# Kernel optimization log

Hardware: AMD Instinct MI355X
Metric: run time of the kernel (lower is better)

The kernel has to match this reference:

```python
import jax, jax.numpy as jnp
import numpy as np

B, S, D, H = 64, 512, 544, 1024  # batch, seq, state_dim+pb_dim, n_hid


def setup_inputs() -> dict:
    key = jax.random.key(0)
    k_x, k_wih, k_whh, k_bih, k_bhh = jax.random.split(key, 5)
    bound = 1.0 / np.sqrt(H)  # PyTorch LSTM uniform init range
    X = jax.random.normal(k_x, (B, S, D), dtype=jnp.float32)
    W_ih = jax.random.uniform(k_wih, (4 * H, D), jnp.float32, -bound, bound)
    W_hh = jax.random.uniform(k_whh, (4 * H, H), jnp.float32, -bound, bound)
    b_ih = jax.random.uniform(k_bih, (4 * H,), jnp.float32, -bound, bound)
    b_hh = jax.random.uniform(k_bhh, (4 * H,), jnp.float32, -bound, bound)
    return {"X": X, "W_ih": W_ih, "W_hh": W_hh, "b_ih": b_ih, "b_hh": b_hh}


def reference(X, W_ih, W_hh, b_ih, b_hh):
    # Faithful to PBRNN.forward: LSTM scanned over the sequence dim
    # (the torch code loops one timestep at a time; the math is a plain
    # single-layer LSTM from zero initial state). Returns final (h, c)
    # stacked as [2, B, H] — the only state forward() produces.
    n_batch = X.shape[0]
    n_hid = W_hh.shape[1]
    Xs = jnp.swapaxes(X, 0, 1)  # [S, B, D]
    # Precompute input projections for all timesteps: [S, B, 4H]
    x_proj = jnp.einsum('sbd,gd->sbg', Xs, W_ih) + (b_ih + b_hh)

    def step(carry, xp):
        h, c = carry
        gates = xp + h @ W_hh.T  # [B, 4H]
        i, f, g, o = jnp.split(gates, 4, axis=-1)  # PyTorch gate order i,f,g,o
        i = jax.nn.sigmoid(i)
        f = jax.nn.sigmoid(f)
        g = jnp.tanh(g)
        o = jax.nn.sigmoid(o)
        c = f * c + i * g
        h = o * jnp.tanh(c)
        return (h, c), None

    h0 = jnp.zeros((n_batch, n_hid), dtype=X.dtype)
    c0 = jnp.zeros((n_batch, n_hid), dtype=X.dtype)
    (h_n, c_n), _ = jax.lax.scan(step, (h0, c0), x_proj)
    return jnp.stack([h_n, c_n])  # [2, B, H]
```

## Files before the change

kernel.cpp:

```cpp
#include <hip/hip_runtime.h>
#include <hip/hip_bf16.h>


#define B_  64
#define S_  512
#define D_  544
#define H_  1024
#define CG_ 64
#define BG_ 4
#define GRID_ (CG_*BG_)

typedef __attribute__((ext_vector_type(8))) short bf16x8;
typedef __attribute__((ext_vector_type(4))) float f32x4;

__device__ inline ushort f2b(float x){
  unsigned u = __float_as_uint(x);
  u = (u + 0x7FFFu + ((u >> 16) & 1u)) >> 16;
  return (ushort)u;
}

__device__ inline bf16x8 pack8(float4 a, float4 b){
  bf16x8 r;
  r[0]=(short)f2b(a.x); r[1]=(short)f2b(a.y); r[2]=(short)f2b(a.z); r[3]=(short)f2b(a.w);
  r[4]=(short)f2b(b.x); r[5]=(short)f2b(b.y); r[6]=(short)f2b(b.z); r[7]=(short)f2b(b.w);
  return r;
}

__device__ inline unsigned long long ld64a(const unsigned long long* q){
  return __hip_atomic_load(q, __ATOMIC_RELAXED, __HIP_MEMORY_SCOPE_AGENT);
}

__device__ inline float sigm(float x){ return __builtin_amdgcn_rcpf(1.f + __expf(-x)); }
__device__ inline float tanh_(float x){ return 1.f - 2.f*__builtin_amdgcn_rcpf(1.f + __expf(2.f*x)); }

__global__ void cvt_x(const float* __restrict__ x, ushort* __restrict__ xb, int n4){
  int i = blockIdx.x*256 + threadIdx.x;
  if (i >= n4) return;
  float4 v = ((const float4*)x)[i];
  ushort4 o;
  o.x=f2b(v.x); o.y=f2b(v.y); o.z=f2b(v.z); o.w=f2b(v.w);
  ((ushort4*)xb)[i] = o;
}

__global__ __launch_bounds__(256,1) void lstm_persist(
    const float* __restrict__ Wih, const float* __restrict__ Whh,
    const float* __restrict__ bih, const float* __restrict__ bhh,
    const ushort* __restrict__ Xb,
    unsigned* thbuf,
    float* __restrict__ out)
{
  const int tid  = threadIdx.x;
  const int wave = tid >> 6;
  const int lane = tid & 63;
  const int c16  = lane & 15;
  const int quad = lane >> 4;
  const int cg   = blockIdx.x & (CG_-1);
  const int bg   = blockIdx.x >> 6;

  __shared__ float gates_s[4][64][17];

  bf16x8 whhf[4][8];
  #pragma unroll
  for (int mt = 0; mt < 4; ++mt){
    const size_t grow = (size_t)(mt*H_ + cg*16 + c16);
    #pragma unroll
    for (int i = 0; i < 8; ++i){
      int k = wave*256 + i*32 + quad*8;
      const float4* p = (const float4*)(Whh + grow*H_ + k);
      whhf[mt][i] = pack8(p[0], p[1]);
    }
  }
  bf16x8 wihf[4][5];
  #pragma unroll
  for (int mt = 0; mt < 4; ++mt){
    const size_t grow = (size_t)(mt*H_ + cg*16 + c16);
    #pragma unroll
    for (int ii = 0; ii < 5; ++ii){
      int it = wave + 4*ii;
      if (it < 17){
        int k = it*32 + quad*8;
        const float4* p = (const float4*)(Wih + grow*D_ + k);
        wihf[mt][ii] = pack8(p[0], p[1]);
      }
    }
  }

  const int uu = tid & 15;
  const int nn = tid >> 4;
  float bsum[4];
  #pragma unroll
  for (int g = 0; g < 4; ++g)
    bsum[g] = bih[g*H_ + cg*16 + uu] + bhh[g*H_ + cg*16 + uu];
  float cstate = 0.f;

  f32x4 acc[4];

  auto zacc = [&]{
    #pragma unroll
    for (int mt = 0; mt < 4; ++mt) acc[mt] = (f32x4){0.f,0.f,0.f,0.f};
  };
  auto xp_gemm = [&](int t){
    #pragma unroll
    for (int ii = 0; ii < 5; ++ii){
      int it = wave + 4*ii;
      if (it < 17){
        int k = it*32 + quad*8;
        bf16x8 b = *(const bf16x8*)(Xb + ((size_t)(bg*16 + c16)*S_ + t)*D_ + k);
        #pragma unroll
        for (int mt = 0; mt < 4; ++mt)
          acc[mt] = __builtin_amdgcn_mfma_f32_16x16x32_bf16(wihf[mt][ii], b, acc[mt], 0,0,0);
      }
    }
  };

  zacc();
  xp_gemm(0);

  const int obase = (bg*64 + wave*16 + (quad>>1))*256 + c16*16 + (quad&1)*8;

  for (int t = 0; t < S_; ++t){
    const unsigned* hp = thbuf + (t & 1) * (B_*H_);
    unsigned*       hn = thbuf + ((t & 1) ^ 1) * (B_*H_);

    {
      const unsigned tag = (unsigned)t & 0xffffu;
      const unsigned long long tmask = 0xffff0000ffff0000ull;
      const unsigned long long texp  = ((unsigned long long)tag << 16)
                                     | ((unsigned long long)tag << 48);
      unsigned long long q[8][4];
      #pragma unroll
      for (int i = 0; i < 8; ++i){
        const unsigned long long* p = (const unsigned long long*)(hp + obase + i*512);
        q[i][0] = ld64a(p);   q[i][1] = ld64a(p+1);
        q[i][2] = ld64a(p+2); q[i][3] = ld64a(p+3);
      }
      #pragma unroll
      for (int i = 0; i < 8; ++i){
        const unsigned long long* p = (const unsigned long long*)(hp + obase + i*512);
        long guard = 0;
        while ((((q[i][0]^texp)|(q[i][1]^texp)|(q[i][2]^texp)|(q[i][3]^texp)) & tmask) != 0ull){
          q[i][0] = ld64a(p);   q[i][1] = ld64a(p+1);
          q[i][2] = ld64a(p+2); q[i][3] = ld64a(p+3);
          if (++guard > (1L<<20)) break;
        }
        union { unsigned u[4]; bf16x8 v8; } eb;
        #pragma unroll
        for (int w = 0; w < 4; ++w){
          unsigned lo = (unsigned)q[i][w];
          unsigned hi = (unsigned)(q[i][w] >> 32);
          eb.u[w] = (lo & 0xffffu) | (hi << 16);
        }
        #pragma unroll
        for (int mt = 0; mt < 4; ++mt)
          acc[mt] = __builtin_amdgcn_mfma_f32_16x16x32_bf16(whhf[mt][i], eb.v8, acc[mt], 0,0,0);
      }
    }

    #pragma unroll
    for (int mt = 0; mt < 4; ++mt)
      #pragma unroll
      for (int r = 0; r < 4; ++r)
        gates_s[wave][mt*16 + quad*4 + r][c16] = acc[mt][r];
    __syncthreads();

    {
      float gsum[4];
      #pragma unroll
      for (int g = 0; g < 4; ++g){
        float s = bsum[g];
        #pragma unroll
        for (int q2 = 0; q2 < 4; ++q2) s += gates_s[q2][g*16 + uu][nn];
        gsum[g] = s;
      }
      float iv = sigm(gsum[0]), fv = sigm(gsum[1]), gv = tanh_(gsum[2]), ov = sigm(gsum[3]);
      float cn = fv*cstate + iv*gv;
      cstate = cn;
      float hv = ov*tanh_(cn);
      unsigned word = (((unsigned)(t+1) & 0xffffu) << 16) | (unsigned)f2b(hv);
      __hip_atomic_store(hn + (size_t)(bg*64 + cg)*256 + tid, word,
                         __ATOMIC_RELAXED, __HIP_MEMORY_SCOPE_AGENT);
      if (t == S_-1){
        out[(bg*16 + nn)*H_ + cg*16 + uu]          = hv;
        out[B_*H_ + (bg*16 + nn)*H_ + cg*16 + uu]  = cn;
      }
    }
    __syncthreads();

    if (t < S_-1){
      zacc();
      xp_gemm(t+1);
    }
  }
}

extern "C" void kernel_launch(void* const* d_in, const int* in_sizes, int n_in,
                              void* d_out, int out_size, void* d_ws, size_t ws_size,
                              hipStream_t stream) {
  const float* X   = (const float*)d_in[0];
  const float* Wih = (const float*)d_in[1];
  const float* Whh = (const float*)d_in[2];
  const float* bih = (const float*)d_in[3];
  const float* bhh = (const float*)d_in[4];
  float* out = (float*)d_out;

  char* ws = (char*)d_ws;
  const size_t THBUF_BYTES = 2ull * B_ * H_ * sizeof(unsigned);
  const size_t XB_OFF      = THBUF_BYTES;
  const size_t XB_BYTES    = (size_t)B_ * S_ * D_ * sizeof(ushort);
  if (ws_size < XB_OFF + XB_BYTES) return;

  unsigned* thbuf = (unsigned*)ws;
  ushort*   Xb    = (ushort*)(ws + XB_OFF);

  hipMemsetAsync(d_ws, 0, THBUF_BYTES, stream);

  int n4 = B_*S_*D_/4;
  cvt_x<<<(n4 + 255)/256, 256, 0, stream>>>(X, Xb, n4);
  lstm_persist<<<GRID_, 256, 0, stream>>>(Wih, Whh, bih, bhh, Xb, thbuf, out);
}
```

Measured before the change: 2.709 ms.

## Split LSTM into chunked input-projection GEMM and 512-block recurrent kernel

```diff
diff --git a/kernel.cpp b/kernel.cpp
--- a/kernel.cpp
+++ b/kernel.cpp
@@ -6,191 +6,252 @@
 #define S_  512
 #define D_  544
 #define H_  1024
-#define CG_ 64
-#define BG_ 4
-#define GRID_ (CG_*BG_)
 
 typedef __attribute__((ext_vector_type(8))) short bf16x8;
 typedef __attribute__((ext_vector_type(4))) float f32x4;
+typedef __attribute__((ext_vector_type(4))) unsigned int u32x4;
 
 __device__ inline ushort f2b(float x){
   unsigned u = __float_as_uint(x);
   u = (u + 0x7FFFu + ((u >> 16) & 1u)) >> 16;
   return (ushort)u;
 }
-
 __device__ inline bf16x8 pack8(float4 a, float4 b){
   bf16x8 r;
   r[0]=(short)f2b(a.x); r[1]=(short)f2b(a.y); r[2]=(short)f2b(a.z); r[3]=(short)f2b(a.w);
   r[4]=(short)f2b(b.x); r[5]=(short)f2b(b.y); r[6]=(short)f2b(b.z); r[7]=(short)f2b(b.w);
   return r;
 }
-
 __device__ inline unsigned long long ld64a(const unsigned long long* q){
   return __hip_atomic_load(q, __ATOMIC_RELAXED, __HIP_MEMORY_SCOPE_AGENT);
 }
-
 __device__ inline float sigm(float x){ return __builtin_amdgcn_rcpf(1.f + __expf(-x)); }
 __device__ inline float tanh_(float x){ return 1.f - 2.f*__builtin_amdgcn_rcpf(1.f + __expf(2.f*x)); }
-
-__global__ void cvt_x(const float* __restrict__ x, ushort* __restrict__ xb, int n4){
+__device__ inline float b2f(ushort u){ return __uint_as_float(((unsigned)u) << 16); }
+
+__global__ void cvt_bf16(const float* __restrict__ x, ushort* __restrict__ o, int n4){
   int i = blockIdx.x*256 + threadIdx.x;
   if (i >= n4) return;
   float4 v = ((const float4*)x)[i];
-  ushort4 o;
-  o.x=f2b(v.x); o.y=f2b(v.y); o.z=f2b(v.z); o.w=f2b(v.w);
-  ((ushort4*)xb)[i] = o;
-}
-
-__global__ __launch_bounds__(256,1) void lstm_persist(
-    const float* __restrict__ Wih, const float* __restrict__ Whh,
-    const float* __restrict__ bih, const float* __restrict__ bhh,
-    const ushort* __restrict__ Xb,
+  ushort4 r; r.x=f2b(v.x); r.y=f2b(v.y); r.z=f2b(v.z); r.w=f2b(v.w);
+  ((ushort4*)o)[i] = r;
+}
+
+template<bool XB>
+__global__ void xp_gemm(const float* __restrict__ X, const ushort* __restrict__ Xbb,
+                        const ushort* __restrict__ Wihb,
+                        const float* __restrict__ bih, const float* __restrict__ bhh,
+                        ushort* __restrict__ xpb, int t0, int C, int lg){
+  const int tid = threadIdx.x, w = tid>>6, lane = tid&63;
+  const int c16 = lane&15, quad = lane>>4;
+  const int mach = blockIdx.x & 7;
+  const int idx2 = blockIdx.x >> 3;
+  const int cg   = idx2 & 63;
+  const int rblk = idx2 >> 6;
+
+  const int r  = rblk*64 + w*16 + c16;
+  const int bl = r >> lg, ct = r & (C-1);
+  const size_t rowg = ((size_t)(mach*8 + bl)*S_ + (size_t)(t0 + ct));
+
+  f32x4 acc[4];
+  #pragma unroll
+  for (int mt=0; mt<4; ++mt) acc[mt] = (f32x4){0.f,0.f,0.f,0.f};
+
+  for (int it=0; it<17; ++it){
+    bf16x8 bfr;
+    if (XB){
+      bfr = *(const bf16x8*)(Xbb + rowg*D_ + it*32 + quad*8);
+    } else {
+      const float4* p = (const float4*)(X + rowg*D_ + it*32 + quad*8);
+      bfr = pack8(p[0], p[1]);
+    }
+    #pragma unroll
+    for (int mt=0; mt<4; ++mt){
+      bf16x8 afr = *(const bf16x8*)(Wihb + (size_t)(mt*H_ + cg*16 + c16)*D_ + it*32 + quad*8);
+      acc[mt] = __builtin_amdgcn_mfma_f32_16x16x32_bf16(afr, bfr, acc[mt], 0,0,0);
+    }
+  }
+
+  __shared__ ushort lds_ep[4][16][64];
+  #pragma unroll
+  for (int mt=0; mt<4; ++mt)
+    #pragma unroll
+    for (int rg=0; rg<4; ++rg){
+      int uu = quad*4 + rg;
+      int j  = mt*H_ + cg*16 + uu;
+      lds_ep[w][c16][uu*4 + mt] = f2b(acc[mt][rg] + bih[j] + bhh[j]);
+    }
+  __syncthreads();
+
+  {
+    const int rl = lane >> 2, ck = lane & 3;
+    const int r2 = rblk*64 + w*16 + rl;
+    const int bl2 = r2 >> lg, ct2 = r2 & (C-1);
+    const uint4* src = (const uint4*)&lds_ep[w][rl][ck*16];
+    uint4* dst = (uint4*)(xpb + ((((size_t)(mach*64+cg)*C + ct2)*8 + bl2)*64 + ck*16));
+    dst[0] = src[0];
+    dst[1] = src[1];
+  }
+}
+
+__global__ __launch_bounds__(256,2) void lstm_persist(
+    const ushort* __restrict__ Whhb,
+    const ushort* __restrict__ xpb,
     unsigned* thbuf,
-    float* __restrict__ out)
+    float* cws,
+    float* __restrict__ out, int t0, int C)
 {
   const int tid  = threadIdx.x;
   const int wave = tid >> 6;
   const int lane = tid & 63;
   const int c16  = lane & 15;
   const int quad = lane >> 4;
-  const int cg   = blockIdx.x & (CG_-1);
-  const int bg   = blockIdx.x >> 6;
-
-  __shared__ float gates_s[4][64][17];
+  const int mach = blockIdx.x & 7;
+  const int cg   = blockIdx.x >> 3;
+
+  __shared__ float gates_s[2][4][64][9];
 
   bf16x8 whhf[4][8];
   #pragma unroll
-  for (int mt = 0; mt < 4; ++mt){
-    const size_t grow = (size_t)(mt*H_ + cg*16 + c16);
-    #pragma unroll
-    for (int i = 0; i < 8; ++i){
-      int k = wave*256 + i*32 + quad*8;
-      const float4* p = (const float4*)(Whh + grow*H_ + k);
-      whhf[mt][i] = pack8(p[0], p[1]);
-    }
-  }
-  bf16x8 wihf[4][5];
-  #pragma unroll
-  for (int mt = 0; mt < 4; ++mt){
-    const size_t grow = (size_t)(mt*H_ + cg*16 + c16);
-    #pragma unroll
-    for (int ii = 0; ii < 5; ++ii){
-      int it = wave + 4*ii;
-      if (it < 17){
-        int k = it*32 + quad*8;
-        const float4* p = (const float4*)(Wih + grow*D_ + k);
-        wihf[mt][ii] = pack8(p[0], p[1]);
+  for (int mt=0; mt<4; ++mt)
+    #pragma unroll
+    for (int i=0; i<8; ++i)
+      whhf[mt][i] = *(const bf16x8*)(Whhb + (size_t)(mt*H_ + cg*16 + c16)*H_
+                                     + wave*256 + i*32 + quad*8);
+
+  const int uu = tid & 15, nn = (tid >> 4) & 7;
+  float cst = 0.f;
+  if (t0 > 0 && tid < 128) cst = cws[(mach*64+cg)*128 + tid];
+
+  const ushort* xq = xpb + (size_t)(mach*64+cg)*C*512;
+  ushort4 xpv = {0,0,0,0};
+  if (tid < 128) xpv = *(const ushort4*)(xq + (size_t)nn*64 + uu*4);
+
+  const unsigned lo_off = ((unsigned)((wave*32 + quad)*64 + (c16&7)*8)) * 4u;
+
+  for (int t = t0; t < t0 + C; ++t){
+    const char* hp = (const char*)(thbuf + ((size_t)((t&1)*8 + mach) * 8192)) + lo_off;
+    unsigned*   hn = thbuf + ((size_t)(((t+1)&1)*8 + mach) * 8192);
+
+    u32x4 q[16];
+    const unsigned T = ((unsigned)t & 0xffffu) << 16;
+
+    bool good = false;
+    for (int rnd = 0; rnd < 3 && !good; ++rnd){
+      const char* b1 = hp + 4096;
+      asm volatile(
+        "global_load_dwordx4 %0,  %16, off sc0\n\t"
+        "global_load_dwordx4 %1,  %16, off offset:16 sc0\n\t"
+        "global_load_dwordx4 %2,  %16, off offset:1024 sc0\n\t"
+        "global_load_dwordx4 %3,  %16, off offset:1040 sc0\n\t"
+        "global_load_dwordx4 %4,  %16, off offset:2048 sc0\n\t"
+        "global_load_dwordx4 %5,  %16, off offset:2064 sc0\n\t"
+        "global_load_dwordx4 %6,  %16, off offset:3072 sc0\n\t"
+        "global_load_dwordx4 %7,  %16, off offset:3088 sc0\n\t"
+        "global_load_dwordx4 %8,  %17, off sc0\n\t"
+        "global_load_dwordx4 %9,  %17, off offset:16 sc0\n\t"
+        "global_load_dwordx4 %10, %17, off offset:1024 sc0\n\t"
+        "global_load_dwordx4 %11, %17, off offset:1040 sc0\n\t"
+        "global_load_dwordx4 %12, %17, off offset:2048 sc0\n\t"
+        "global_load_dwordx4 %13, %17, off offset:2064 sc0\n\t"
+        "global_load_dwordx4 %14, %17, off offset:3072 sc0\n\t"
+        "global_load_dwordx4 %15, %17, off offset:3088 sc0\n\t"
+        "s_waitcnt vmcnt(0)"
+        : "=v"(q[0]), "=v"(q[1]), "=v"(q[2]),  "=v"(q[3]),
+          "=v"(q[4]), "=v"(q[5]), "=v"(q[6]),  "=v"(q[7]),
+          "=v"(q[8]), "=v"(q[9]), "=v"(q[10]), "=v"(q[11]),
+          "=v"(q[12]),"=v"(q[13]),"=v"(q[14]), "=v"(q[15])
+        : "v"(hp), "v"(b1)
+        : "memory");
+      unsigned bad = 0u;
+      #pragma unroll
+      for (int i=0; i<16; ++i)
+        bad |= ((q[i].x^T)|(q[i].y^T)|(q[i].z^T)|(q[i].w^T)) & 0xffff0000u;
+      good = __all(bad == 0u);
+    }
+    if (!good){
+      unsigned stale = 0u;
+      #pragma unroll
+      for (int i=0; i<16; ++i){
+        unsigned d = ((q[i].x^T)|(q[i].y^T)|(q[i].z^T)|(q[i].w^T)) & 0xffff0000u;
+        stale |= (d != 0u) ? (1u<<i) : 0u;
       }
-    }
-  }
-
-  const int uu = tid & 15;
-  const int nn = tid >> 4;
-  float bsum[4];
-  #pragma unroll
-  for (int g = 0; g < 4; ++g)
-    bsum[g] = bih[g*H_ + cg*16 + uu] + bhh[g*H_ + cg*16 + uu];
-  float cstate = 0.f;
-
-  f32x4 acc[4];
-
-  auto zacc = [&]{
-    #pragma unroll
-    for (int mt = 0; mt < 4; ++mt) acc[mt] = (f32x4){0.f,0.f,0.f,0.f};
-  };
-  auto xp_gemm = [&](int t){
-    #pragma unroll
-    for (int ii = 0; ii < 5; ++ii){
-      int it = wave + 4*ii;
-      if (it < 17){
-        int k = it*32 + quad*8;
-        bf16x8 b = *(const bf16x8*)(Xb + ((size_t)(bg*16 + c16)*S_ + t)*D_ + k);
+      int guard = 0;
+      while (__any(stale != 0u)){
+        unsigned ns = 0u;
         #pragma unroll
-        for (int mt = 0; mt < 4; ++mt)
-          acc[mt] = __builtin_amdgcn_mfma_f32_16x16x32_bf16(wihf[mt][ii], b, acc[mt], 0,0,0);
+        for (int i=0; i<16; ++i){
+          if (stale & (1u<<i)){
+            const unsigned long long* pq =
+              (const unsigned long long*)(hp + (i>>1)*1024 + (i&1)*16);
+            unsigned long long a = ld64a(pq), b = ld64a(pq+1);
+            q[i].x=(unsigned)a; q[i].y=(unsigned)(a>>32);
+            q[i].z=(unsigned)b; q[i].w=(unsigned)(b>>32);
+            unsigned d = ((q[i].x^T)|(q[i].y^T)|(q[i].z^T)|(q[i].w^T)) & 0xffff0000u;
+            ns |= (d != 0u) ? (1u<<i) : 0u;
+          }
+        }
+        stale = ns;
+        if (++guard > 8192) break;
+        __builtin_amdgcn_s_sleep(1);
       }
     }
-  };
-
-  zacc();
-  xp_gemm(0);
-
-  const int obase = (bg*64 + wave*16 + (quad>>1))*256 + c16*16 + (quad&1)*8;
-
-  for (int t = 0; t < S_; ++t){
-    const unsigned* hp = thbuf + (t & 1) * (B_*H_);
-    unsigned*       hn = thbuf + ((t & 1) ^ 1) * (B_*H_);
-
-    {
-      const unsigned tag = (unsigned)t & 0xffffu;
-      const unsigned long long tmask = 0xffff0000ffff0000ull;
-      const unsigned long long texp  = ((unsigned long long)tag << 16)
-                                     | ((unsigned long long)tag << 48);
-      unsigned long long q[8][4];
-      #pragma unroll
-      for (int i = 0; i < 8; ++i){
-        const unsigned long long* p = (const unsigned long long*)(hp + obase + i*512);
-        q[i][0] = ld64a(p);   q[i][1] = ld64a(p+1);
-        q[i][2] = ld64a(p+2); q[i][3] = ld64a(p+3);
-      }
-      #pragma unroll
-      for (int i = 0; i < 8; ++i){
-        const unsigned long long* p = (const unsigned long long*)(hp + obase + i*512);
-        long guard = 0;
-        while ((((q[i][0]^texp)|(q[i][1]^texp)|(q[i][2]^texp)|(q[i][3]^texp)) & tmask) != 0ull){
-          q[i][0] = ld64a(p);   q[i][1] = ld64a(p+1);
-          q[i][2] = ld64a(p+2); q[i][3] = ld64a(p+3);
-          if (++guard > (1L<<20)) break;
-        }
-        union { unsigned u[4]; bf16x8 v8; } eb;
+
+    f32x4 acc[4];
+    #pragma unroll
+    for (int mt=0; mt<4; ++mt) acc[mt] = (f32x4){0.f,0.f,0.f,0.f};
+    #pragma unroll
+    for (int f=0; f<8; ++f){
+      union { unsigned u[4]; bf16x8 v8; } eb;
+      eb.u[0] = __builtin_amdgcn_perm(q[2*f].y,   q[2*f].x,   0x05040100u);
+      eb.u[1] = __builtin_amdgcn_perm(q[2*f].w,   q[2*f].z,   0x05040100u);
+      eb.u[2] = __builtin_amdgcn_perm(q[2*f+1].y, q[2*f+1].x, 0x05040100u);
+      eb.u[3] = __builtin_amdgcn_perm(q[2*f+1].w, q[2*f+1].z, 0x05040100u);
+      #pragma unroll
+      for (int mt=0; mt<4; ++mt)
+        acc[mt] = __builtin_amdgcn_mfma_f32_16x16x32_bf16(whhf[mt][f], eb.v8, acc[mt], 0,0,0);
+    }
+
+    if (c16 < 8){
+      #pragma unroll
+      for (int mt=0; mt<4; ++mt)
         #pragma unroll
-        for (int w = 0; w < 4; ++w){
-          unsigned lo = (unsigned)q[i][w];
-          unsigned hi = (unsigned)(q[i][w] >> 32);
-          eb.u[w] = (lo & 0xffffu) | (hi << 16);
-        }
-        #pragma unroll
-        for (int mt = 0; mt < 4; ++mt)
-          acc[mt] = __builtin_amdgcn_mfma_f32_16x16x32_bf16(whhf[mt][i], eb.v8, acc[mt], 0,0,0);
-      }
-    }
-
-    #pragma unroll
-    for (int mt = 0; mt < 4; ++mt)
-      #pragma unroll
-      for (int r = 0; r < 4; ++r)
-        gates_s[wave][mt*16 + quad*4 + r][c16] = acc[mt][r];
+        for (int rg=0; rg<4; ++rg)
+          gates_s[t&1][wave][mt*16 + quad*4 + rg][c16] = acc[mt][rg];
+    }
     __syncthreads();
 
-    {
+    if (tid < 128){
       float gsum[4];
       #pragma unroll
-      for (int g = 0; g < 4; ++g){
-        float s = bsum[g];
-        #pragma unroll
-        for (int q2 = 0; q2 < 4; ++q2) s += gates_s[q2][g*16 + uu][nn];
+      for (int g=0; g<4; ++g){
+        float s;
+        s  = gates_s[t&1][0][g*16+uu][nn];
+        s += gates_s[t&1][1][g*16+uu][nn];
+        s += gates_s[t&1][2][g*16+uu][nn];
+        s += gates_s[t&1][3][g*16+uu][nn];
         gsum[g] = s;
       }
+      gsum[0] += b2f(xpv.x); gsum[1] += b2f(xpv.y);
+      gsum[2] += b2f(xpv.z); gsum[3] += b2f(xpv.w);
       float iv = sigm(gsum[0]), fv = sigm(gsum[1]), gv = tanh_(gsum[2]), ov = sigm(gsum[3]);
-      float cn = fv*cstate + iv*gv;
-      cstate = cn;
+      float cn = fv*cst + iv*gv;
+      cst = cn;
       float hv = ov*tanh_(cn);
-      unsigned word = (((unsigned)(t+1) & 0xffffu) << 16) | (unsigned)f2b(hv);
-      __hip_atomic_store(hn + (size_t)(bg*64 + cg)*256 + tid, word,
-                         __ATOMIC_RELAXED, __HIP_MEMORY_SCOPE_AGENT);
+      unsigned word = (((unsigned)(t+1)) << 16) | (unsigned)f2b(hv);
+      unsigned* wp = hn + (cg*2 + (uu>>3))*64 + nn*8 + (uu&7);
+      asm volatile("global_store_dword %0, %1, off" :: "v"(wp), "v"(word) : "memory");
+      __hip_atomic_store(wp, word, __ATOMIC_RELAXED, __HIP_MEMORY_SCOPE_AGENT);
       if (t == S_-1){
-        out[(bg*16 + nn)*H_ + cg*16 + uu]          = hv;
-        out[B_*H_ + (bg*16 + nn)*H_ + cg*16 + uu]  = cn;
+        out[(mach*8+nn)*H_ + cg*16 + uu]          = hv;
+        out[B_*H_ + (mach*8+nn)*H_ + cg*16 + uu]  = cn;
       }
-    }
-    __syncthreads();
-
-    if (t < S_-1){
-      zacc();
-      xp_gemm(t+1);
+      int ctn = t - t0 + 1; if (ctn >= C) ctn = C-1;
+      xpv = *(const ushort4*)(xq + (size_t)ctn*512 + (size_t)nn*64 + uu*4);
     }
   }
+
+  if (tid < 128) cws[(mach*64+cg)*128 + tid] = cst;
 }
 
 extern "C" void kernel_launch(void* const* d_in, const int* in_sizes, int n_in,
@@ -204,17 +265,39 @@
   float* out = (float*)d_out;
 
   char* ws = (char*)d_ws;
-  const size_t THBUF_BYTES = 2ull * B_ * H_ * sizeof(unsigned);
-  const size_t XB_OFF      = THBUF_BYTES;
-  const size_t XB_BYTES    = (size_t)B_ * S_ * D_ * sizeof(ushort);
-  if (ws_size < XB_OFF + XB_BYTES) return;
-
-  unsigned* thbuf = (unsigned*)ws;
-  ushort*   Xb    = (ushort*)(ws + XB_OFF);
-
-  hipMemsetAsync(d_ws, 0, THBUF_BYTES, stream);
-
-  int n4 = B_*S_*D_/4;
-  cvt_x<<<(n4 + 255)/256, 256, 0, stream>>>(X, Xb, n4);
-  lstm_persist<<<GRID_, 256, 0, stream>>>(Wih, Whh, bih, bhh, Xb, thbuf, out);
-}
+  const size_t OFF_TH = 0, OFF_CWS = 524288, OFF_WIH = 786432, OFF_WHH = 5242880;
+  const size_t OFF_XPB = 13631488;
+  const size_t XB_BYTES = 35651584;
+
+  int C = 0, lg = 0, useXb = 0;
+  if      (ws_size >= OFF_XPB + 524288ull*64 + XB_BYTES){ C=64; lg=6; useXb=1; }
+  else if (ws_size >= OFF_XPB + 524288ull*32 + XB_BYTES){ C=32; lg=5; useXb=1; }
+  else if (ws_size >= OFF_XPB + 524288ull*16 + XB_BYTES){ C=16; lg=4; useXb=1; }
+  else if (ws_size >= OFF_XPB + 524288ull*32)           { C=32; lg=5; useXb=0; }
+  else if (ws_size >= OFF_XPB + 524288ull*16)           { C=16; lg=4; useXb=0; }
+  else return;
+
+  unsigned* thbuf = (unsigned*)(ws + OFF_TH);
+  float*    cws   = (float*)(ws + OFF_CWS);
+  ushort*   Wihb  = (ushort*)(ws + OFF_WIH);
+  ushort*   Whhb  = (ushort*)(ws + OFF_WHH);
+  ushort*   xpb   = (ushort*)(ws + OFF_XPB);
+  ushort*   Xb    = (ushort*)(ws + OFF_XPB + 524288ull*C);
+
+  hipMemsetAsync(d_ws, 0, OFF_WIH, stream);
+
+  cvt_bf16<<<(4096*544/4 + 255)/256, 256, 0, stream>>>(Wih, Wihb, 4096*544/4);
+  cvt_bf16<<<(4096*1024/4 + 255)/256, 256, 0, stream>>>(Whh, Whhb, 4096*1024/4);
+  if (useXb)
+    cvt_bf16<<<(B_*S_*D_/4 + 255)/256, 256, 0, stream>>>(X, Xb, B_*S_*D_/4);
+
+  const int nch = S_ / C;
+  for (int ch = 0; ch < nch; ++ch){
+    const int t0 = ch * C;
+    if (useXb)
+      xp_gemm<true ><<<64*C, 256, 0, stream>>>(X, Xb, Wihb, bih, bhh, xpb, t0, C, lg);
+    else
+      xp_gemm<false><<<64*C, 256, 0, stream>>>(X, Xb, Wihb, bih, bhh, xpb, t0, C, lg);
+    lstm_persist<<<512, 256, 0, stream>>>(Whhb, xpb, thbuf, cws, out, t0, C);
+  }
+}
```

Measured after the change: 4.514 ms. 1.67x slower.
